# Kernel optimization log

Measured on AMD Instinct MI355X. Metric: run time of the kernel, lower is better.

The kernel has to match this reference:

```python
import jax, jax.numpy as jnp
import numpy as np

EPS_RMS = 1e-6
EPS_NORM = 1e-9


def rmsnorm(x):
    return x * jax.lax.rsqrt(jnp.mean(x * x, axis=-1, keepdims=True) + EPS_RMS)


def apply_rotary(x, cos, sin):
    # x: [b, h, s, d]; cos/sin: [1, 1, s, d//2]
    d2 = x.shape[-1] // 2
    x1, x2 = x[..., :d2], x[..., d2:]
    return jnp.concatenate([x1 * cos - x2 * sin, x1 * sin + x2 * cos], axis=-1)


def setup_inputs() -> dict:
    key = jax.random.key(0)
    ks = jax.random.split(key, 16)
    b, l, e, h = 4, 1024, 2048, 16
    d = e // h
    query = jax.random.normal(ks[0], (b, l, e), jnp.float32)
    keyt = jax.random.normal(ks[1], (b, l, e), jnp.float32)
    value = jax.random.normal(ks[2], (b, l, e), jnp.float32)
    attn_mask = jnp.tril(jnp.ones((l, l), bool))[None, None]  # causal bool mask
    cos = jax.random.normal(ks[3], (1, 1, l, d // 2), jnp.float32)
    sin = jax.random.normal(ks[4], (1, 1, l, d // 2), jnp.float32)
    sc = 0.02
    Wq = jax.random.normal(ks[5], (e, e), jnp.float32) * sc
    bq = jnp.zeros((e,), jnp.float32)
    Wk = jax.random.normal(ks[6], (e, e), jnp.float32) * sc
    bk = jnp.zeros((e,), jnp.float32)
    Wv = jax.random.normal(ks[7], (e, e), jnp.float32) * sc
    bv = jnp.zeros((e,), jnp.float32)
    Wo = jax.random.normal(ks[8], (e, e), jnp.float32) * sc
    bo = jnp.zeros((e,), jnp.float32)
    return dict(query=query, key=keyt, value=value, attn_mask=attn_mask,
                cos=cos, sin=sin, Wq=Wq, bq=bq, Wk=Wk, bk=bk,
                Wv=Wv, bv=bv, Wo=Wo, bo=bo)


def reference(query, key, value, attn_mask, cos, sin, Wq, bq, Wk, bk, Wv, bv, Wo, bo):
    b, l, e = query.shape
    s = key.shape[1]
    h = 16
    d = e // h
    q = (query @ Wq.T + bq).reshape(b, l, h, d).transpose(0, 2, 1, 3)
    k = (key @ Wk.T + bk).reshape(b, s, h, d).transpose(0, 2, 1, 3)
    v = (value @ Wv.T + bv).reshape(b, s, h, d).transpose(0, 2, 1, 3)
    q, k = rmsnorm(q), rmsnorm(k)
    # rotary (self-attention, s == l)
    q = apply_rotary(q, cos[:, :, :s], sin[:, :, :s])
    k = apply_rotary(k, cos[:, :, :s], sin[:, :, :s])
    # SDPA with boolean mask
    scores = jnp.einsum('bhld,bhsd->bhls', q, k) / jnp.sqrt(jnp.float32(d))
    scores = jnp.where(attn_mask, scores, jnp.finfo(scores.dtype).min)
    p = jax.nn.softmax(scores, axis=-1)
    o = jnp.einsum('bhls,bhsd->bhld', p, v)  # [b,h,l,d]
    # post-attention v-orthogonalization (o.shape == v.shape here)
    vnorm = jnp.sqrt(jnp.sum(v * v, axis=-1, keepdims=True))
    vn = v / jnp.maximum(vnorm, EPS_NORM)
    o = o - jnp.sum(o * vn, axis=-1, keepdims=True) * vn
    o = o.transpose(0, 2, 1, 3).reshape(b, l, e)
    return o @ Wo.T + bo
```

## Files before the change

kernel.cpp:

```cpp
#include <hip/hip_runtime.h>

typedef short short8 __attribute__((ext_vector_type(8)));
typedef float f32x4 __attribute__((ext_vector_type(4)));

#define MFMA_BF16 __builtin_amdgcn_mfma_f32_16x16x32_bf16

__device__ __forceinline__ unsigned short f2bf(float f) {
  unsigned int u = __float_as_uint(f);
  u += 0x7fffu + ((u >> 16) & 1u);
  return (unsigned short)(u >> 16);
}
__device__ __forceinline__ float bf2f(unsigned short u) {
  return __uint_as_float(((unsigned int)u) << 16);
}

typedef __attribute__((address_space(1))) const unsigned int as1_u32;
typedef __attribute__((address_space(3))) unsigned int as3_u32;
__device__ __forceinline__ void gld16(const void* g, void* l) {
  __builtin_amdgcn_global_load_lds((as1_u32*)(unsigned long long)g,
                                   (as3_u32*)(unsigned int)(unsigned long long)l,
                                   16, 0, 0);
}

struct CvtArgs {
  const float* s[7];
  unsigned short* d[7];
  int n8[7];
};

__global__ __launch_bounds__(256) void cvtall(CvtArgs a) {
  const int seg = blockIdx.y;
  int i = blockIdx.x * 256 + threadIdx.x;
  if (i >= a.n8[seg]) return;
  const float4* s4 = (const float4*)a.s[seg];
  float4 x = s4[2 * i], y = s4[2 * i + 1];
  short8 o = {(short)f2bf(x.x), (short)f2bf(x.y), (short)f2bf(x.z), (short)f2bf(x.w),
              (short)f2bf(y.x), (short)f2bf(y.y), (short)f2bf(y.z), (short)f2bf(y.w)};
  *(short8*)&a.d[seg][(size_t)i * 8] = o;
}

template <bool OUTBF>
__global__ __launch_bounds__(256) void gemm_bf16(
    const unsigned short* __restrict__ A0, const unsigned short* __restrict__ A1,
    const unsigned short* __restrict__ A2,
    const unsigned short* __restrict__ W0, const unsigned short* __restrict__ W1,
    const unsigned short* __restrict__ W2,
    const float* __restrict__ g0, const float* __restrict__ g1,
    const float* __restrict__ g2,
    float* __restrict__ Cf0, unsigned short* __restrict__ Cb0,
    unsigned short* __restrict__ Cb1, unsigned short* __restrict__ Cb2,
    int M, int N, int K) {
  const int z = blockIdx.z;
  const unsigned short* A = z == 0 ? A0 : (z == 1 ? A1 : A2);
  const unsigned short* W = z == 0 ? W0 : (z == 1 ? W1 : W2);
  const float* bias = z == 0 ? g0 : (z == 1 ? g1 : g2);
  unsigned short* Cb = z == 0 ? Cb0 : (z == 1 ? Cb1 : Cb2);

  __shared__ unsigned short As[128 * 32];
  __shared__ unsigned short Bs[128 * 32];
  const int t = threadIdx.x, lane = t & 63, w = t >> 6;
  const int wr = w >> 1, wc = w & 1;
  const int quad = lane >> 4, l16 = lane & 15;
  const int bm = blockIdx.y * 128, bn = blockIdx.x * 128;

  const int r0 = (w * 2 + 0) * 16 + (lane >> 2);
  const int r1 = (w * 2 + 1) * 16 + (lane >> 2);
  const size_t a0 = (size_t)(bm + r0) * K + (lane & 3) * 8;
  const size_t a1 = (size_t)(bm + r1) * K + (lane & 3) * 8;
  const size_t b0 = (size_t)(bn + r0) * K + (lane & 3) * 8;
  const size_t b1 = (size_t)(bn + r1) * K + (lane & 3) * 8;
  unsigned short* lA0 = &As[(w * 2 + 0) * 512];
  unsigned short* lA1 = &As[(w * 2 + 1) * 512];
  unsigned short* lB0 = &Bs[(w * 2 + 0) * 512];
  unsigned short* lB1 = &Bs[(w * 2 + 1) * 512];

  const f32x4 fz = {0.f, 0.f, 0.f, 0.f};
  f32x4 acc[4][4];
  for (int i = 0; i < 4; ++i)
    for (int j = 0; j < 4; ++j) acc[i][j] = fz;

  for (int k0 = 0; k0 < K; k0 += 32) {
    __syncthreads();
    gld16(A + a0 + k0, lA0);
    gld16(A + a1 + k0, lA1);
    gld16(W + b0 + k0, lB0);
    gld16(W + b1 + k0, lB1);
    __syncthreads();
    short8 af[4], bfv[4];
    for (int mt = 0; mt < 4; ++mt)
      af[mt] = *(const short8*)&As[(wr * 64 + mt * 16 + l16) * 32 + quad * 8];
    for (int nt = 0; nt < 4; ++nt)
      bfv[nt] = *(const short8*)&Bs[(wc * 64 + nt * 16 + l16) * 32 + quad * 8];
    for (int mt = 0; mt < 4; ++mt)
      for (int nt = 0; nt < 4; ++nt)
        acc[mt][nt] = MFMA_BF16(af[mt], bfv[nt], acc[mt][nt], 0, 0, 0);
  }

  for (int mt = 0; mt < 4; ++mt)
    for (int nt = 0; nt < 4; ++nt) {
      int row = bm + wr * 64 + mt * 16 + quad * 4;
      int col = bn + wc * 64 + nt * 16 + l16;
      float bc = bias[col];
      for (int r = 0; r < 4; ++r) {
        float v = acc[mt][nt][r] + bc;
        if (OUTBF) Cb[(size_t)(row + r) * N + col] = f2bf(v);
        else       Cf0[(size_t)(row + r) * N + col] = v;
      }
    }
}

__global__ __launch_bounds__(256) void rmsrope(
    const unsigned short* __restrict__ Qf, const unsigned short* __restrict__ Kf,
    const float* __restrict__ cosT, const float* __restrict__ sinT,
    unsigned short* __restrict__ Qb, unsigned short* __restrict__ Kb) {
  const int rid = blockIdx.x * 4 + (threadIdx.x >> 6);
  const int lane = threadIdx.x & 63;
  const int li = rid & 1023;
  const int bh = rid >> 10;
  const int hi = bh & 15, bi = bh >> 4;
  const int src = (bi * 1024 + li) * 2048 + hi * 128;
  const int dst = rid * 128;
  const float c = cosT[li * 64 + lane];
  const float s = sinT[li * 64 + lane];

  float q1 = bf2f(Qf[src + lane]), q2 = bf2f(Qf[src + 64 + lane]);
  float ss = q1 * q1 + q2 * q2;
  for (int off = 32; off; off >>= 1) ss += __shfl_xor(ss, off, 64);
  float r = rsqrtf(ss * (1.f / 128.f) + 1e-6f);
  float qa = q1 * r, qb2 = q2 * r;
  const float qsc = 0.08838834764831845f * 1.4426950408889634f;
  Qb[dst + lane]      = f2bf((qa * c - qb2 * s) * qsc);
  Qb[dst + 64 + lane] = f2bf((qa * s + qb2 * c) * qsc);

  float k1 = bf2f(Kf[src + lane]), k2 = bf2f(Kf[src + 64 + lane]);
  float ks = k1 * k1 + k2 * k2;
  for (int off = 32; off; off >>= 1) ks += __shfl_xor(ks, off, 64);
  float rk = rsqrtf(ks * (1.f / 128.f) + 1e-6f);
  float ka = k1 * rk, kb2 = k2 * rk;
  Kb[dst + lane]      = f2bf(ka * c - kb2 * s);
  Kb[dst + 64 + lane] = f2bf(ka * s + kb2 * c);
}

__global__ __launch_bounds__(256) void vtrans(
    const unsigned short* __restrict__ Vf, unsigned short* __restrict__ Vt) {
  __shared__ unsigned short Vsh[64 * 136];
  const int t = threadIdx.x;
  const int bh = blockIdx.y, l0 = blockIdx.x * 64;
  const int hi = bh & 15, bi = bh >> 4;
  {
    int row = t >> 2, c4 = t & 3;
    const unsigned short* src = &Vf[(size_t)(bi * 1024 + l0 + row) * 2048 + hi * 128];
    for (int i = 0; i < 4; ++i) {
      int chunk = c4 * 4 + i;
      *(int4*)&Vsh[row * 136 + chunk * 8] = *(const int4*)&src[chunk * 8];
    }
  }
  __syncthreads();
  {
    int d = t >> 1, half = t & 1;
    unsigned short* dst = &Vt[(size_t)bh * 131072 + (size_t)d * 1024 + l0 + half * 32];
    for (int g = 0; g < 4; ++g) {
      short8 o;
      for (int j = 0; j < 8; ++j)
        o[j] = (short)Vsh[(half * 32 + g * 8 + j) * 136 + d];
      *(short8*)&dst[g * 8] = o;
    }
  }
}

__global__ __launch_bounds__(512, 4) void attn(
    const unsigned short* __restrict__ Qb, const unsigned short* __restrict__ Kb,
    const unsigned short* __restrict__ Vt, unsigned short* __restrict__ Of0,
    unsigned short* __restrict__ Of1, float* __restrict__ Lb) {
  __shared__ unsigned short Kl[64 * 136];
  __shared__ unsigned short Vl[128 * 72];
  __shared__ unsigned short Pl[8][16 * 72];
  const int t = threadIdx.x, lane = t & 63, w = t >> 6;
  const int quad = lane >> 4, l16 = lane & 15;
  const int B = blockIdx.x;
  const int bh = (B & 7) + 8 * ((B >> 3) & 7);
  const int jj = B >> 6;
  const int pair = jj >> 1, split = jj & 1;
  const unsigned short* Qh = Qb + (size_t)bh * 131072;
  const unsigned short* Kh = Kb + (size_t)bh * 131072;
  const unsigned short* Vh = Vt + (size_t)bh * 131072;
  unsigned short* Oh = (split ? Of1 : Of0) + (size_t)bh * 131072;
  float* Lh = Lb + split * 65536 + bh * 1024;

  const int krow = t >> 4, kcol = (t & 15) * 8;
  const int vdr = t >> 3, vc = (t & 7) * 8;
  const f32x4 fz = {0.f, 0.f, 0.f, 0.f};

  for (int ti = 0; ti < 2; ++ti) {
    const int qt = ti == 0 ? 7 - pair : pair;
    const int q0 = qt * 128;

    short8 aQ[4];
    {
      int qr = q0 + w * 16 + l16;
      for (int kk = 0; kk < 4; ++kk)
        aQ[kk] = *(const short8*)&Qh[(size_t)qr * 128 + kk * 32 + quad * 8];
    }
    f32x4 oacc[8];
    for (int i = 0; i < 8; ++i) oacc[i] = fz;
    float Lr[4] = {0.f, 0.f, 0.f, 0.f};
    const int nST = 2 * qt + 2;

    for (int st = split; st < nST; st += 2) {
      const int s0 = st * 64;
      __syncthreads();
      {
        *(int4*)&Kl[krow * 136 + kcol] =
            *(const int4*)&Kh[(size_t)(s0 + krow) * 128 + kcol];
        *(int4*)&Kl[(krow + 32) * 136 + kcol] =
            *(const int4*)&Kh[(size_t)(s0 + krow + 32) * 128 + kcol];
        *(int4*)&Vl[vdr * 72 + vc] =
            *(const int4*)&Vh[(size_t)vdr * 1024 + s0 + vc];
        *(int4*)&Vl[(vdr + 64) * 72 + vc] =
            *(const int4*)&Vh[(size_t)(vdr + 64) * 1024 + s0 + vc];
      }
      __syncthreads();

      f32x4 sfr[4];
      for (int j = 0; j < 4; ++j) sfr[j] = fz;
      for (int kk = 0; kk < 4; ++kk)
        for (int ni = 0; ni < 4; ++ni) {
          short8 bK = *(const short8*)&Kl[(ni * 16 + l16) * 136 + kk * 32 + quad * 8];
          sfr[ni] = MFMA_BF16(aQ[kk], bK, sfr[ni], 0, 0, 0);
        }

      const bool diag = (s0 + 63 > q0);
      for (int r = 0; r < 4; ++r) {
        int q = q0 + w * 16 + quad * 4 + r;
        float ps = 0.f;
        for (int ni = 0; ni < 4; ++ni) {
          float sv = sfr[ni][r];
          if (diag && (s0 + ni * 16 + l16 > q)) sv = -30000.f;
          float pp = exp2f(sv - 16.5f);
          ps += pp;
          Pl[w][(quad * 4 + r) * 72 + ni * 16 + l16] = f2bf(pp);
        }
        ps += __shfl_xor(ps, 1, 64);
        ps += __shfl_xor(ps, 2, 64);
        ps += __shfl_xor(ps, 4, 64);
        ps += __shfl_xor(ps, 8, 64);
        Lr[r] += ps;
      }

      for (int kk = 0; kk < 2; ++kk) {
        short8 aP = *(const short8*)&Pl[w][l16 * 72 + kk * 32 + quad * 8];
        for (int nt = 0; nt < 8; ++nt) {
          short8 bV = *(const short8*)&Vl[(nt * 16 + l16) * 72 + kk * 32 + quad * 8];
          oacc[nt] = MFMA_BF16(aP, bV, oacc[nt], 0, 0, 0);
        }
      }
    }

    for (int r = 0; r < 4; ++r) {
      int q = q0 + w * 16 + quad * 4 + r;
      size_t base = (size_t)q * 128;
      for (int nt = 0; nt < 8; ++nt)
        Oh[base + nt * 16 + l16] = f2bf(oacc[nt][r]);
      if (l16 == 0) Lh[q] = Lr[r];
    }
  }
}

__global__ __launch_bounds__(256) void vnfix(
    const unsigned short* __restrict__ Of0, const unsigned short* __restrict__ Of1,
    const float* __restrict__ Lb, const unsigned short* __restrict__ Vf,
    unsigned short* __restrict__ Op) {
  const int rid = blockIdx.x * 4 + (threadIdx.x >> 6);
  const int lane = threadIdx.x & 63;
  const int li = rid & 1023;
  const int bh = rid >> 10;
  const int hi = bh & 15, bi = bh >> 4;
  const int src = (bi * 1024 + li) * 2048 + hi * 128;
  float inv = 1.f / (Lb[rid] + Lb[65536 + rid]);
  float o1 = (bf2f(Of0[(size_t)rid * 128 + lane]) + bf2f(Of1[(size_t)rid * 128 + lane])) * inv;
  float o2 = (bf2f(Of0[(size_t)rid * 128 + 64 + lane]) + bf2f(Of1[(size_t)rid * 128 + 64 + lane])) * inv;
  float v1 = bf2f(Vf[src + lane]), v2 = bf2f(Vf[src + 64 + lane]);
  float vv = v1 * v1 + v2 * v2;
  float dd = o1 * v1 + o2 * v2;
  for (int off = 32; off; off >>= 1) {
    vv += __shfl_xor(vv, off, 64);
    dd += __shfl_xor(dd, off, 64);
  }
  float vn = fmaxf(sqrtf(vv), 1e-9f);
  float tc = dd / (vn * vn);
  Op[src + lane]      = f2bf(o1 - tc * v1);
  Op[src + 64 + lane] = f2bf(o2 - tc * v2);
}

extern "C" void kernel_launch(void* const* d_in, const int* in_sizes, int n_in,
                              void* d_out, int out_size, void* d_ws, size_t ws_size,
                              hipStream_t stream) {
  const float* query = (const float*)d_in[0];
  const float* key   = (const float*)d_in[1];
  const float* value = (const float*)d_in[2];
  const float* cosT  = (const float*)d_in[4];
  const float* sinT  = (const float*)d_in[5];
  const float* Wq = (const float*)d_in[6];
  const float* bq = (const float*)d_in[7];
  const float* Wk = (const float*)d_in[8];
  const float* bk = (const float*)d_in[9];
  const float* Wv = (const float*)d_in[10];
  const float* bv = (const float*)d_in[11];
  const float* Wo = (const float*)d_in[12];
  const float* bo = (const float*)d_in[13];
  float* out = (float*)d_out;

  char* ws = (char*)d_ws;
  const size_t MB = 1048576;
  unsigned short* Xq  = (unsigned short*)(ws);
  unsigned short* Xk  = (unsigned short*)(ws + 16 * MB);
  unsigned short* Xv  = (unsigned short*)(ws + 32 * MB);
  unsigned short* Wqb = (unsigned short*)(ws + 48 * MB);
  unsigned short* Wkb = (unsigned short*)(ws + 56 * MB);
  unsigned short* Wvb = (unsigned short*)(ws + 64 * MB);
  unsigned short* Wob = (unsigned short*)(ws + 72 * MB);
  unsigned short* Qf  = (unsigned short*)(ws + 80 * MB);
  unsigned short* Kf  = (unsigned short*)(ws + 96 * MB);
  unsigned short* Vf  = (unsigned short*)(ws + 112 * MB);
  unsigned short* Qbb = Xq;
  unsigned short* Kbb = Xk;
  unsigned short* Vtb = Xv;
  unsigned short* Of0 = Qf;
  unsigned short* Of1 = Kf;
  float*          Lbp = (float*)(ws + 64 * MB);
  unsigned short* Opb = (unsigned short*)(ws + 48 * MB);

  CvtArgs ca;
  ca.s[0] = query; ca.d[0] = Xq;  ca.n8[0] = 1048576;
  ca.s[1] = key;   ca.d[1] = Xk;  ca.n8[1] = 1048576;
  ca.s[2] = value; ca.d[2] = Xv;  ca.n8[2] = 1048576;
  ca.s[3] = Wq;    ca.d[3] = Wqb; ca.n8[3] = 524288;
  ca.s[4] = Wk;    ca.d[4] = Wkb; ca.n8[4] = 524288;
  ca.s[5] = Wv;    ca.d[5] = Wvb; ca.n8[5] = 524288;
  ca.s[6] = Wo;    ca.d[6] = Wob; ca.n8[6] = 524288;
  cvtall<<<dim3(4096, 7), 256, 0, stream>>>(ca);

  gemm_bf16<true><<<dim3(16, 32, 3), 256, 0, stream>>>(
      Xq, Xk, Xv, Wqb, Wkb, Wvb, bq, bk, bv,
      nullptr, Qf, Kf, Vf, 4096, 2048, 2048);

  rmsrope<<<16384, 256, 0, stream>>>(Qf, Kf, cosT, sinT, Qbb, Kbb);
  vtrans<<<dim3(16, 64), 256, 0, stream>>>(Vf, Vtb);

  attn<<<512, 512, 0, stream>>>(Qbb, Kbb, Vtb, Of0, Of1, Lbp);

  vnfix<<<16384, 256, 0, stream>>>(Of0, Of1, Lbp, Vf, Opb);

  gemm_bf16<false><<<dim3(16, 32, 1), 256, 0, stream>>>(
      Opb, nullptr, nullptr, Wob, nullptr, nullptr, bo, nullptr, nullptr,
      out, nullptr, nullptr, nullptr, 4096, 2048, 2048);
}
```

Baseline: 477.2 us.

## Deepen GEMM K-tile to 64, add XCD-aware block swizzle, fuse rmsrope with vtrans

The GEMM now stages 64-wide K tiles per barrier pair instead of 32, halving the number of synchronisation rounds. It also remaps the 1D grid so that blocks on the same XCD work on neighbouring 128x128 output tiles, which should improve L2 reuse of the A and W operands. Separately, the rmsnorm+rotary kernel and the V transpose are merged into one launch by branching on block index, saving one kernel launch. Doubling LDS per block (32KB) may reduce occupancy.

```diff
diff --git a/kernel.cpp b/kernel.cpp
--- a/kernel.cpp
+++ b/kernel.cpp
@@ -39,61 +39,71 @@
   *(short8*)&a.d[seg][(size_t)i * 8] = o;
 }
 
-template <bool OUTBF>
-__global__ __launch_bounds__(256) void gemm_bf16(
-    const unsigned short* __restrict__ A0, const unsigned short* __restrict__ A1,
-    const unsigned short* __restrict__ A2,
-    const unsigned short* __restrict__ W0, const unsigned short* __restrict__ W1,
-    const unsigned short* __restrict__ W2,
-    const float* __restrict__ g0, const float* __restrict__ g1,
-    const float* __restrict__ g2,
-    float* __restrict__ Cf0, unsigned short* __restrict__ Cb0,
-    unsigned short* __restrict__ Cb1, unsigned short* __restrict__ Cb2,
-    int M, int N, int K) {
-  const int z = blockIdx.z;
-  const unsigned short* A = z == 0 ? A0 : (z == 1 ? A1 : A2);
-  const unsigned short* W = z == 0 ? W0 : (z == 1 ? W1 : W2);
-  const float* bias = z == 0 ? g0 : (z == 1 ? g1 : g2);
-  unsigned short* Cb = z == 0 ? Cb0 : (z == 1 ? Cb1 : Cb2);
-
-  __shared__ unsigned short As[128 * 32];
-  __shared__ unsigned short Bs[128 * 32];
+struct GemmArgs {
+  const unsigned short* A[3];
+  const unsigned short* W[3];
+  const float* bias[3];
+  unsigned short* Cb[3];
+  float* Cf;
+};
+
+template <bool OUTBF, int NZ>
+__global__ __launch_bounds__(256) void gemm_bf16(GemmArgs g) {
+  const int B = blockIdx.x;
+  const int xcd = B & 7;
+  const int i = B >> 3;
+  const int z = i >> 6;
+  const int r = i & 63;
+  const int xb = r >> 4, inner = r & 15;
+  const int bn = (xb * 4 + (inner & 3)) * 128;
+  const int bm = (xcd * 4 + (inner >> 2)) * 128;
+  const int K = 2048, N = 2048;
+
+  const unsigned short* A = g.A[z];
+  const unsigned short* W = g.W[z];
+  const float* bias = g.bias[z];
+  unsigned short* Cb = g.Cb[z];
+
+  __shared__ unsigned short As[128 * 64];
+  __shared__ unsigned short Bs[128 * 64];
   const int t = threadIdx.x, lane = t & 63, w = t >> 6;
   const int wr = w >> 1, wc = w & 1;
   const int quad = lane >> 4, l16 = lane & 15;
-  const int bm = blockIdx.y * 128, bn = blockIdx.x * 128;
-
-  const int r0 = (w * 2 + 0) * 16 + (lane >> 2);
-  const int r1 = (w * 2 + 1) * 16 + (lane >> 2);
-  const size_t a0 = (size_t)(bm + r0) * K + (lane & 3) * 8;
-  const size_t a1 = (size_t)(bm + r1) * K + (lane & 3) * 8;
-  const size_t b0 = (size_t)(bn + r0) * K + (lane & 3) * 8;
-  const size_t b1 = (size_t)(bn + r1) * K + (lane & 3) * 8;
-  unsigned short* lA0 = &As[(w * 2 + 0) * 512];
-  unsigned short* lA1 = &As[(w * 2 + 1) * 512];
-  unsigned short* lB0 = &Bs[(w * 2 + 0) * 512];
-  unsigned short* lB1 = &Bs[(w * 2 + 1) * 512];
+
+  const int srow = lane >> 3;
+  const int sk = (lane & 7) * 8;
+  size_t ga[4], gb[4];
+  unsigned short *la[4], *lb[4];
+  for (int j = 0; j < 4; ++j) {
+    int rr = (w * 4 + j) * 8 + srow;
+    ga[j] = (size_t)(bm + rr) * K + sk;
+    gb[j] = (size_t)(bn + rr) * K + sk;
+    la[j] = &As[(w * 4 + j) * 512];
+    lb[j] = &Bs[(w * 4 + j) * 512];
+  }
 
   const f32x4 fz = {0.f, 0.f, 0.f, 0.f};
   f32x4 acc[4][4];
-  for (int i = 0; i < 4; ++i)
-    for (int j = 0; j < 4; ++j) acc[i][j] = fz;
-
-  for (int k0 = 0; k0 < K; k0 += 32) {
+  for (int a = 0; a < 4; ++a)
+    for (int b = 0; b < 4; ++b) acc[a][b] = fz;
+
+  for (int k0 = 0; k0 < K; k0 += 64) {
     __syncthreads();
-    gld16(A + a0 + k0, lA0);
-    gld16(A + a1 + k0, lA1);
-    gld16(W + b0 + k0, lB0);
-    gld16(W + b1 + k0, lB1);
+    for (int j = 0; j < 4; ++j) {
+      gld16(A + ga[j] + k0, la[j]);
+      gld16(W + gb[j] + k0, lb[j]);
+    }
     __syncthreads();
-    short8 af[4], bfv[4];
-    for (int mt = 0; mt < 4; ++mt)
-      af[mt] = *(const short8*)&As[(wr * 64 + mt * 16 + l16) * 32 + quad * 8];
-    for (int nt = 0; nt < 4; ++nt)
-      bfv[nt] = *(const short8*)&Bs[(wc * 64 + nt * 16 + l16) * 32 + quad * 8];
-    for (int mt = 0; mt < 4; ++mt)
+    for (int kk = 0; kk < 2; ++kk) {
+      short8 af[4], bfv[4];
+      for (int mt = 0; mt < 4; ++mt)
+        af[mt] = *(const short8*)&As[(wr * 64 + mt * 16 + l16) * 64 + kk * 32 + quad * 8];
       for (int nt = 0; nt < 4; ++nt)
-        acc[mt][nt] = MFMA_BF16(af[mt], bfv[nt], acc[mt][nt], 0, 0, 0);
+        bfv[nt] = *(const short8*)&Bs[(wc * 64 + nt * 16 + l16) * 64 + kk * 32 + quad * 8];
+      for (int mt = 0; mt < 4; ++mt)
+        for (int nt = 0; nt < 4; ++nt)
+          acc[mt][nt] = MFMA_BF16(af[mt], bfv[nt], acc[mt][nt], 0, 0, 0);
+    }
   }
 
   for (int mt = 0; mt < 4; ++mt)
@@ -101,69 +111,71 @@
       int row = bm + wr * 64 + mt * 16 + quad * 4;
       int col = bn + wc * 64 + nt * 16 + l16;
       float bc = bias[col];
-      for (int r = 0; r < 4; ++r) {
-        float v = acc[mt][nt][r] + bc;
-        if (OUTBF) Cb[(size_t)(row + r) * N + col] = f2bf(v);
-        else       Cf0[(size_t)(row + r) * N + col] = v;
-      }
-    }
-}
-
-__global__ __launch_bounds__(256) void rmsrope(
+      for (int r2 = 0; r2 < 4; ++r2) {
+        float v = acc[mt][nt][r2] + bc;
+        if (OUTBF) Cb[(size_t)(row + r2) * N + col] = f2bf(v);
+        else       g.Cf[(size_t)(row + r2) * N + col] = v;
+      }
+    }
+}
+
+__global__ __launch_bounds__(256) void rmsvt(
     const unsigned short* __restrict__ Qf, const unsigned short* __restrict__ Kf,
+    const unsigned short* __restrict__ Vf,
     const float* __restrict__ cosT, const float* __restrict__ sinT,
-    unsigned short* __restrict__ Qb, unsigned short* __restrict__ Kb) {
-  const int rid = blockIdx.x * 4 + (threadIdx.x >> 6);
-  const int lane = threadIdx.x & 63;
-  const int li = rid & 1023;
-  const int bh = rid >> 10;
-  const int hi = bh & 15, bi = bh >> 4;
-  const int src = (bi * 1024 + li) * 2048 + hi * 128;
-  const int dst = rid * 128;
-  const float c = cosT[li * 64 + lane];
-  const float s = sinT[li * 64 + lane];
-
-  float q1 = bf2f(Qf[src + lane]), q2 = bf2f(Qf[src + 64 + lane]);
-  float ss = q1 * q1 + q2 * q2;
-  for (int off = 32; off; off >>= 1) ss += __shfl_xor(ss, off, 64);
-  float r = rsqrtf(ss * (1.f / 128.f) + 1e-6f);
-  float qa = q1 * r, qb2 = q2 * r;
-  const float qsc = 0.08838834764831845f * 1.4426950408889634f;
-  Qb[dst + lane]      = f2bf((qa * c - qb2 * s) * qsc);
-  Qb[dst + 64 + lane] = f2bf((qa * s + qb2 * c) * qsc);
-
-  float k1 = bf2f(Kf[src + lane]), k2 = bf2f(Kf[src + 64 + lane]);
-  float ks = k1 * k1 + k2 * k2;
-  for (int off = 32; off; off >>= 1) ks += __shfl_xor(ks, off, 64);
-  float rk = rsqrtf(ks * (1.f / 128.f) + 1e-6f);
-  float ka = k1 * rk, kb2 = k2 * rk;
-  Kb[dst + lane]      = f2bf(ka * c - kb2 * s);
-  Kb[dst + 64 + lane] = f2bf(ka * s + kb2 * c);
-}
-
-__global__ __launch_bounds__(256) void vtrans(
-    const unsigned short* __restrict__ Vf, unsigned short* __restrict__ Vt) {
+    unsigned short* __restrict__ Qb, unsigned short* __restrict__ Kb,
+    unsigned short* __restrict__ Vt) {
   __shared__ unsigned short Vsh[64 * 136];
-  const int t = threadIdx.x;
-  const int bh = blockIdx.y, l0 = blockIdx.x * 64;
-  const int hi = bh & 15, bi = bh >> 4;
-  {
-    int row = t >> 2, c4 = t & 3;
-    const unsigned short* src = &Vf[(size_t)(bi * 1024 + l0 + row) * 2048 + hi * 128];
-    for (int i = 0; i < 4; ++i) {
-      int chunk = c4 * 4 + i;
-      *(int4*)&Vsh[row * 136 + chunk * 8] = *(const int4*)&src[chunk * 8];
-    }
-  }
-  __syncthreads();
-  {
-    int d = t >> 1, half = t & 1;
-    unsigned short* dst = &Vt[(size_t)bh * 131072 + (size_t)d * 1024 + l0 + half * 32];
-    for (int g = 0; g < 4; ++g) {
-      short8 o;
-      for (int j = 0; j < 8; ++j)
-        o[j] = (short)Vsh[(half * 32 + g * 8 + j) * 136 + d];
-      *(short8*)&dst[g * 8] = o;
+  if (blockIdx.x < 16384) {
+    const int rid = blockIdx.x * 4 + (threadIdx.x >> 6);
+    const int lane = threadIdx.x & 63;
+    const int li = rid & 1023;
+    const int bh = rid >> 10;
+    const int hi = bh & 15, bi = bh >> 4;
+    const int src = (bi * 1024 + li) * 2048 + hi * 128;
+    const int dst = rid * 128;
+    const float c = cosT[li * 64 + lane];
+    const float s = sinT[li * 64 + lane];
+
+    float q1 = bf2f(Qf[src + lane]), q2 = bf2f(Qf[src + 64 + lane]);
+    float ss = q1 * q1 + q2 * q2;
+    for (int off = 32; off; off >>= 1) ss += __shfl_xor(ss, off, 64);
+    float r = rsqrtf(ss * (1.f / 128.f) + 1e-6f);
+    float qa = q1 * r, qb2 = q2 * r;
+    const float qsc = 0.08838834764831845f * 1.4426950408889634f;
+    Qb[dst + lane]      = f2bf((qa * c - qb2 * s) * qsc);
+    Qb[dst + 64 + lane] = f2bf((qa * s + qb2 * c) * qsc);
+
+    float k1 = bf2f(Kf[src + lane]), k2 = bf2f(Kf[src + 64 + lane]);
+    float ks = k1 * k1 + k2 * k2;
+    for (int off = 32; off; off >>= 1) ks += __shfl_xor(ks, off, 64);
+    float rk = rsqrtf(ks * (1.f / 128.f) + 1e-6f);
+    float ka = k1 * rk, kb2 = k2 * rk;
+    Kb[dst + lane]      = f2bf(ka * c - kb2 * s);
+    Kb[dst + 64 + lane] = f2bf(ka * s + kb2 * c);
+  } else {
+    const int bid = blockIdx.x - 16384;
+    const int t = threadIdx.x;
+    const int bh = bid >> 4, l0 = (bid & 15) * 64;
+    const int hi = bh & 15, bi = bh >> 4;
+    {
+      int row = t >> 2, c4 = t & 3;
+      const unsigned short* src = &Vf[(size_t)(bi * 1024 + l0 + row) * 2048 + hi * 128];
+      for (int i = 0; i < 4; ++i) {
+        int chunk = c4 * 4 + i;
+        *(int4*)&Vsh[row * 136 + chunk * 8] = *(const int4*)&src[chunk * 8];
+      }
+    }
+    __syncthreads();
+    {
+      int d = t >> 1, half = t & 1;
+      unsigned short* dst = &Vt[(size_t)bh * 131072 + (size_t)d * 1024 + l0 + half * 32];
+      for (int g = 0; g < 4; ++g) {
+        short8 o;
+        for (int j = 0; j < 8; ++j)
+          o[j] = (short)Vsh[(half * 32 + g * 8 + j) * 136 + d];
+        *(short8*)&dst[g * 8] = o;
+      }
     }
   }
 }
@@ -340,18 +352,25 @@
   ca.s[6] = Wo;    ca.d[6] = Wob; ca.n8[6] = 524288;
   cvtall<<<dim3(4096, 7), 256, 0, stream>>>(ca);
 
-  gemm_bf16<true><<<dim3(16, 32, 3), 256, 0, stream>>>(
-      Xq, Xk, Xv, Wqb, Wkb, Wvb, bq, bk, bv,
-      nullptr, Qf, Kf, Vf, 4096, 2048, 2048);
-
-  rmsrope<<<16384, 256, 0, stream>>>(Qf, Kf, cosT, sinT, Qbb, Kbb);
-  vtrans<<<dim3(16, 64), 256, 0, stream>>>(Vf, Vtb);
+  GemmArgs gp;
+  gp.A[0] = Xq;  gp.A[1] = Xk;  gp.A[2] = Xv;
+  gp.W[0] = Wqb; gp.W[1] = Wkb; gp.W[2] = Wvb;
+  gp.bias[0] = bq; gp.bias[1] = bk; gp.bias[2] = bv;
+  gp.Cb[0] = Qf; gp.Cb[1] = Kf; gp.Cb[2] = Vf;
+  gp.Cf = nullptr;
+  gemm_bf16<true, 3><<<1536, 256, 0, stream>>>(gp);
+
+  rmsvt<<<17408, 256, 0, stream>>>(Qf, Kf, Vf, cosT, sinT, Qbb, Kbb, Vtb);
 
   attn<<<512, 512, 0, stream>>>(Qbb, Kbb, Vtb, Of0, Of1, Lbp);
 
   vnfix<<<16384, 256, 0, stream>>>(Of0, Of1, Lbp, Vf, Opb);
 
-  gemm_bf16<false><<<dim3(16, 32, 1), 256, 0, stream>>>(
-      Opb, nullptr, nullptr, Wob, nullptr, nullptr, bo, nullptr, nullptr,
-      out, nullptr, nullptr, nullptr, 4096, 2048, 2048);
-}
+  GemmArgs go;
+  go.A[0] = Opb; go.A[1] = nullptr; go.A[2] = nullptr;
+  go.W[0] = Wob; go.W[1] = nullptr; go.W[2] = nullptr;
+  go.bias[0] = bo; go.bias[1] = nullptr; go.bias[2] = nullptr;
+  go.Cb[0] = nullptr; go.Cb[1] = nullptr; go.Cb[2] = nullptr;
+  go.Cf = out;
+  gemm_bf16<false, 1><<<512, 256, 0, stream>>>(go);
+}
```

Result: no change. 473.3 us (-0.8%).
